# Optimization experiments

Hardware: AMD Instinct MI355X
Metric: run time of the kernel (lower is better)

Reference implementation:

```python
import jax, jax.numpy as jnp
import numpy as np

N, D = 8192, 128
EPS = 1e-6  # torch F.pairwise_distance default eps


def _pe(d, s=3, t=2):
    # 1/d^s - 1/d^t
    return 1.0 / (d ** s) - 1.0 / (d ** t)


def setup_inputs() -> dict:
    key = jax.random.key(0)
    x = jax.random.normal(key, (N, D), dtype=jnp.float32)
    return {"x": x}


def reference(x):
    n = x.shape[0]
    # loss0: distance of each row to the origin; torch pairwise_distance adds eps to the diff
    d0 = jnp.sqrt(jnp.sum((x + EPS) ** 2, axis=-1))  # [N]
    loss0 = jnp.mean(jnp.clip(_pe(d0), -1.5, 1000.0))

    # pdist: condensed upper-triangular pairwise Euclidean distances (no eps)
    sq = jnp.sum(x * x, axis=-1)                      # [N]
    d2 = sq[:, None] + sq[None, :] - 2.0 * (x @ x.T)  # [N, N]
    mask = jnp.triu(jnp.ones((n, n), dtype=bool), k=1)
    # keep masked entries at 1.0 so sqrt/pe stay finite
    d2 = jnp.where(mask, jnp.maximum(d2, 0.0), 1.0)
    d = jnp.sqrt(d2)
    vals = jnp.clip(_pe(d), -1.5, 1000.0)
    cnt = n * (n - 1) // 2
    loss = jnp.sum(jnp.where(mask, vals, 0.0)) / cnt
    return loss0 + loss
```

## Files before the change

kernel.cpp:

```cpp
#include <hip/hip_runtime.h>
#include <hip/hip_bf16.h>


#define NROWS 8192
#define DDIM  128
#define TILE  128
#define RB    128
#define TTILES (NROWS / TILE)
#define NTRI  (TTILES * (TTILES + 1) / 2)
#define NBLKP 1024
#define FEPS  1e-6f

typedef float f32x4 __attribute__((ext_vector_type(4)));
typedef long long i64;

__device__ __forceinline__ float rsq_fast(float x) {
    float r;
    asm("v_rsq_f32 %0, %1" : "=v"(r) : "v"(x));
    return r;
}

__global__ __launch_bounds__(256) void convert_kernel(
        const float* __restrict__ x, unsigned short* __restrict__ xf8_u16,
        float* __restrict__ sq, float* __restrict__ p0) {
    int tid = threadIdx.x;
    int wave = tid >> 6, lane = tid & 63;
    int row = blockIdx.x * 4 + wave;

    float2 v = *(const float2*)(x + (size_t)row * DDIM + lane * 2);
    float s = v.x * v.x + v.y * v.y;
    float ex = v.x + FEPS, ey = v.y + FEPS;
    float e = ex * ex + ey * ey;

    int packed = __builtin_amdgcn_cvt_pk_fp8_f32(v.x, v.y, 0, false);
    xf8_u16[(size_t)row * 64 + lane] = (unsigned short)(packed & 0xFFFF);

    #pragma unroll
    for (int off = 32; off; off >>= 1) {
        s += __shfl_down(s, off);
        e += __shfl_down(e, off);
    }

    __shared__ float red[4];
    if (lane == 0) {
        sq[row] = s;
        float r = rsqrtf(e);
        float r2 = r * r;
        red[wave] = fminf(fmaxf(r2 * r - r2, -1.5f), 1000.0f);
    }
    __syncthreads();
    if (tid == 0) p0[blockIdx.x] = red[0] + red[1] + red[2] + red[3];
}

__device__ __forceinline__ int tri_off(int i) {
    return i * TTILES - ((i * (i - 1)) >> 1);
}

__device__ __forceinline__ void stage_tile(const char* __restrict__ g,
                                           char* lds, int tid) {
    uint4 v[2];
    #pragma unroll
    for (int p = 0; p < 2; ++p)
        v[p] = *(const uint4*)(g + (p * 512 + tid) * 16);
    #pragma unroll
    for (int p = 0; p < 2; ++p) {
        int n = p * 512 + tid;
        int row = n >> 3, c = n & 7;
        *(uint4*)(lds + row * RB + ((c * 16) ^ ((row & 7) << 4))) = v[p];
    }
}

__global__ __launch_bounds__(512, 4) void pair_kernel(
        const unsigned short* __restrict__ xf8_u16,
        const float* __restrict__ sq, float* __restrict__ pp) {
    const char* xb = (const char*)xf8_u16;
    __shared__ char smem[32768];
    char* ldsA = smem;
    char* ldsB = smem + 16384;

    int b = blockIdx.x;
    int t0, cnt;
    if (b < 32) { t0 = b * 3; cnt = 3; }
    else        { t0 = 96 + (b - 32) * 2; cnt = 2; }

    int I = 0;
    {
        float T2 = 2.0f * TTILES + 1.0f;
        I = (int)((T2 - sqrtf(T2 * T2 - 8.0f * (float)t0)) * 0.5f);
        while (tri_off(I + 1) <= t0) ++I;
        while (tri_off(I) > t0) --I;
    }
    int J = I + (t0 - tri_off(I));

    int tid = threadIdx.x;
    int wave = tid >> 6, lane = tid & 63;
    int wR = (wave >> 2) * 64;
    int wC = (wave & 3) * 32;
    int lcol = lane & 15;
    int lrow = lane >> 4;

    float lsum = 0.0f;
    int curI = -1;

    for (int k = 0; k < cnt; ++k) {
        if (I != curI) { stage_tile(xb + (size_t)I * TILE * RB, ldsA, tid); curI = I; }
        bool diag = (I == J);
        if (!diag) stage_tile(xb + (size_t)J * TILE * RB, ldsB, tid);
        __syncthreads();
        const char* bufB = diag ? ldsA : ldsB;

        f32x4 acc[4][2];
        #pragma unroll
        for (int r = 0; r < 4; ++r)
            #pragma unroll
            for (int c = 0; c < 2; ++c) acc[r][c] = (f32x4){0.f, 0.f, 0.f, 0.f};

        #pragma unroll
        for (int ks = 0; ks < 4; ++ks) {
            int koff = ks * 32 + lrow * 8;
            i64 a[4], bb[2];
            #pragma unroll
            for (int r = 0; r < 4; ++r) {
                int row = wR + r * 16 + lcol;
                a[r] = *(const i64*)(ldsA + row * RB + (koff ^ ((row & 7) << 4)));
            }
            #pragma unroll
            for (int c = 0; c < 2; ++c) {
                int row = wC + c * 16 + lcol;
                bb[c] = *(const i64*)(bufB + row * RB + (koff ^ ((row & 7) << 4)));
            }
            #pragma unroll
            for (int r = 0; r < 4; ++r)
                #pragma unroll
                for (int c = 0; c < 2; ++c)
                    acc[r][c] = __builtin_amdgcn_mfma_f32_16x16x32_fp8_fp8(
                        a[r], bb[c], acc[r][c], 0, 0, 0);
        }

        int ibase = I * TILE + wR + lrow * 4;
        int jbase = J * TILE + wC + lcol;
        float sqj[2];
        #pragma unroll
        for (int c = 0; c < 2; ++c) sqj[c] = sq[jbase + c * 16];

        if (!diag) {
            #pragma unroll
            for (int r = 0; r < 4; ++r)
                #pragma unroll
                for (int u = 0; u < 4; ++u) {
                    float si = sq[ibase + r * 16 + u];
                    #pragma unroll
                    for (int c = 0; c < 2; ++c) {
                        float d2 = si + sqj[c] - 2.0f * acc[r][c][u];
                        float rv = rsq_fast(d2);
                        float r2 = rv * rv;
                        lsum += r2 * rv - r2;
                    }
                }
        } else {
            int il0 = wR + lrow * 4;
            int jl0 = wC + lcol;
            #pragma unroll
            for (int r = 0; r < 4; ++r)
                #pragma unroll
                for (int u = 0; u < 4; ++u) {
                    int il = il0 + r * 16 + u;
                    float si = sq[ibase + r * 16 + u];
                    #pragma unroll
                    for (int c = 0; c < 2; ++c) {
                        if (jl0 + c * 16 > il) {
                            float d2 = fmaxf(si + sqj[c] - 2.0f * acc[r][c][u], 1e-30f);
                            float rv = rsq_fast(d2);
                            float r2 = rv * rv;
                            lsum += fminf(r2 * rv - r2, 1000.0f);
                        }
                    }
                }
        }
        __syncthreads();

        ++J;
        if (J == TTILES) { ++I; J = I; }
    }

    #pragma unroll
    for (int off = 32; off; off >>= 1) lsum += __shfl_down(lsum, off);
    __shared__ float red[8];
    if (lane == 0) red[wave] = lsum;
    __syncthreads();
    if (tid == 0) {
        float t = 0.f;
        #pragma unroll
        for (int w = 0; w < 8; ++w) t += red[w];
        pp[blockIdx.x] = t;
    }
}

__global__ __launch_bounds__(1024) void reduce_kernel(
        const float* __restrict__ p0, int n0,
        const float* __restrict__ pp, int np, float* __restrict__ out) {
    int tid = threadIdx.x;
    double s0 = 0.0, sp = 0.0;
    for (int i = tid; i < n0; i += 1024) s0 += (double)p0[i];
    for (int i = tid; i < np; i += 1024) sp += (double)pp[i];
    __shared__ double sh0[1024], shp[1024];
    sh0[tid] = s0; shp[tid] = sp;
    __syncthreads();
    for (int s = 512; s; s >>= 1) {
        if (tid < s) { sh0[tid] += sh0[tid + s]; shp[tid] += shp[tid + s]; }
        __syncthreads();
    }
    if (tid == 0) {
        double cnt = (double)NROWS * (double)(NROWS - 1) * 0.5;
        out[0] = (float)(sh0[0] / (double)NROWS + shp[0] / cnt);
    }
}

extern "C" void kernel_launch(void* const* d_in, const int* in_sizes, int n_in,
                              void* d_out, int out_size, void* d_ws, size_t ws_size,
                              hipStream_t stream) {
    const float* x = (const float*)d_in[0];
    char* ws = (char*)d_ws;
    const size_t OFF_SQ = 1048576;
    const size_t OFF_P0 = OFF_SQ + 32768;
    const size_t OFF_PP = OFF_P0 + 8192;
    if (ws_size < OFF_PP + NBLKP * sizeof(float)) return;

    unsigned short* xf8 = (unsigned short*)ws;
    float* sq = (float*)(ws + OFF_SQ);
    float* p0 = (float*)(ws + OFF_P0);
    float* pp = (float*)(ws + OFF_PP);

    convert_kernel<<<NROWS / 4, 256, 0, stream>>>(x, xf8, sq, p0);
    pair_kernel<<<NBLKP, 512, 0, stream>>>(xf8, sq, pp);
    reduce_kernel<<<1, 1024, 0, stream>>>(p0, NROWS / 4, pp, NBLKP, (float*)d_out);
}
```

Measured before the change: 29.39 us.

## Use packed FP32 math in pair epilogue, hoist row norms, shuffle-based final reduce

The off-diagonal epilogue now uses v_pk_add/fma/mul_f32 to handle two distance values per instruction. It keeps separate accumulators for the r^3 and r^2 sums and combines them only at the end. Row squared norms are loaded once per I tile into registers instead of being reloaded for every element. The final reduction switches from a shared-memory tree with many barriers to wave shuffles plus a small shared array. The goal is fewer VALU instructions and fewer memory loads in the epilogue, at the cost of extra registers and a slightly different summation order.

```diff
diff --git a/kernel.cpp b/kernel.cpp
--- a/kernel.cpp
+++ b/kernel.cpp
@@ -12,12 +12,28 @@
 #define FEPS  1e-6f
 
 typedef float f32x4 __attribute__((ext_vector_type(4)));
+typedef float f32x2 __attribute__((ext_vector_type(2)));
 typedef long long i64;
 
 __device__ __forceinline__ float rsq_fast(float x) {
     float r;
     asm("v_rsq_f32 %0, %1" : "=v"(r) : "v"(x));
     return r;
+}
+__device__ __forceinline__ f32x2 pk_fma(f32x2 a, f32x2 b, f32x2 c) {
+    f32x2 d;
+    asm("v_pk_fma_f32 %0, %1, %2, %3" : "=v"(d) : "v"(a), "v"(b), "v"(c));
+    return d;
+}
+__device__ __forceinline__ f32x2 pk_add(f32x2 a, f32x2 b) {
+    f32x2 d;
+    asm("v_pk_add_f32 %0, %1, %2" : "=v"(d) : "v"(a), "v"(b));
+    return d;
+}
+__device__ __forceinline__ f32x2 pk_mul(f32x2 a, f32x2 b) {
+    f32x2 d;
+    asm("v_pk_mul_f32 %0, %1, %2" : "=v"(d) : "v"(a), "v"(b));
+    return d;
 }
 
 __global__ __launch_bounds__(256) void convert_kernel(
@@ -99,11 +115,25 @@
     int lcol = lane & 15;
     int lrow = lane >> 4;
 
-    float lsum = 0.0f;
+    const f32x2 neg2 = {-2.0f, -2.0f};
+    f32x2 l3 = {0.f, 0.f}, l2 = {0.f, 0.f};
+    float ldiag = 0.0f;
+    f32x2 si2[4][2];
     int curI = -1;
 
     for (int k = 0; k < cnt; ++k) {
-        if (I != curI) { stage_tile(xb + (size_t)I * TILE * RB, ldsA, tid); curI = I; }
+        if (I != curI) {
+            stage_tile(xb + (size_t)I * TILE * RB, ldsA, tid);
+            int ibase = I * TILE + wR + lrow * 4;
+            #pragma unroll
+            for (int r = 0; r < 4; ++r)
+                #pragma unroll
+                for (int h = 0; h < 2; ++h) {
+                    float2 v = *(const float2*)(sq + ibase + r * 16 + h * 2);
+                    si2[r][h] = (f32x2){v.x, v.y};
+                }
+            curI = I;
+        }
         bool diag = (I == J);
         if (!diag) stage_tile(xb + (size_t)J * TILE * RB, ldsB, tid);
         __syncthreads();
@@ -137,26 +167,29 @@
                         a[r], bb[c], acc[r][c], 0, 0, 0);
         }
 
-        int ibase = I * TILE + wR + lrow * 4;
         int jbase = J * TILE + wC + lcol;
         float sqj[2];
         #pragma unroll
         for (int c = 0; c < 2; ++c) sqj[c] = sq[jbase + c * 16];
 
         if (!diag) {
-            #pragma unroll
-            for (int r = 0; r < 4; ++r)
-                #pragma unroll
-                for (int u = 0; u < 4; ++u) {
-                    float si = sq[ibase + r * 16 + u];
+            f32x2 sj2[2];
+            #pragma unroll
+            for (int c = 0; c < 2; ++c) sj2[c] = (f32x2){sqj[c], sqj[c]};
+            #pragma unroll
+            for (int r = 0; r < 4; ++r)
+                #pragma unroll
+                for (int c = 0; c < 2; ++c)
                     #pragma unroll
-                    for (int c = 0; c < 2; ++c) {
-                        float d2 = si + sqj[c] - 2.0f * acc[r][c][u];
-                        float rv = rsq_fast(d2);
-                        float r2 = rv * rv;
-                        lsum += r2 * rv - r2;
+                    for (int h = 0; h < 2; ++h) {
+                        f32x2 acc2 = {acc[r][c][2 * h], acc[r][c][2 * h + 1]};
+                        f32x2 s2 = pk_add(si2[r][h], sj2[c]);
+                        f32x2 d2 = pk_fma(acc2, neg2, s2);
+                        f32x2 rv = {rsq_fast(d2[0]), rsq_fast(d2[1])};
+                        f32x2 r2 = pk_mul(rv, rv);
+                        l3 = pk_fma(r2, rv, l3);
+                        l2 = pk_add(l2, r2);
                     }
-                }
         } else {
             int il0 = wR + lrow * 4;
             int jl0 = wC + lcol;
@@ -165,14 +198,14 @@
                 #pragma unroll
                 for (int u = 0; u < 4; ++u) {
                     int il = il0 + r * 16 + u;
-                    float si = sq[ibase + r * 16 + u];
+                    float si = si2[r][u >> 1][u & 1];
                     #pragma unroll
                     for (int c = 0; c < 2; ++c) {
                         if (jl0 + c * 16 > il) {
                             float d2 = fmaxf(si + sqj[c] - 2.0f * acc[r][c][u], 1e-30f);
                             float rv = rsq_fast(d2);
                             float r2 = rv * rv;
-                            lsum += fminf(r2 * rv - r2, 1000.0f);
+                            ldiag += fminf(r2 * rv - r2, 1000.0f);
                         }
                     }
                 }
@@ -182,6 +215,8 @@
         ++J;
         if (J == TTILES) { ++I; J = I; }
     }
+
+    float lsum = (l3[0] + l3[1]) - (l2[0] + l2[1]) + ldiag;
 
     #pragma unroll
     for (int off = 32; off; off >>= 1) lsum += __shfl_down(lsum, off);
@@ -203,16 +238,21 @@
     double s0 = 0.0, sp = 0.0;
     for (int i = tid; i < n0; i += 1024) s0 += (double)p0[i];
     for (int i = tid; i < np; i += 1024) sp += (double)pp[i];
-    __shared__ double sh0[1024], shp[1024];
-    sh0[tid] = s0; shp[tid] = sp;
+    #pragma unroll
+    for (int off = 32; off; off >>= 1) {
+        s0 += __shfl_down(s0, off);
+        sp += __shfl_down(sp, off);
+    }
+    __shared__ double sh[32];
+    int wave = tid >> 6, lane = tid & 63;
+    if (lane == 0) { sh[2 * wave] = s0; sh[2 * wave + 1] = sp; }
     __syncthreads();
-    for (int s = 512; s; s >>= 1) {
-        if (tid < s) { sh0[tid] += sh0[tid + s]; shp[tid] += shp[tid + s]; }
-        __syncthreads();
-    }
     if (tid == 0) {
+        double a = 0.0, bsum = 0.0;
+        #pragma unroll
+        for (int w = 0; w < 16; ++w) { a += sh[2 * w]; bsum += sh[2 * w + 1]; }
         double cnt = (double)NROWS * (double)(NROWS - 1) * 0.5;
-        out[0] = (float)(sh0[0] / (double)NROWS + shp[0] / cnt);
+        out[0] = (float)(a / (double)NROWS + bsum / cnt);
     }
 }
 
```

Result: faster. 28.59 us (-2.7%).
